# Kernel optimization log

Measured on AMD Instinct MI355X. Metric: run time of the kernel, lower is better.

## Reference

```python
import jax, jax.numpy as jnp
import numpy as np

THRESHOLD = 0.02  # matches init threshold
N_POINTS = 4_000_000
N_PLANES = 64


def setup_inputs() -> dict:
    key = jax.random.key(0)
    k1, k2, k3 = jax.random.split(key, 3)
    points = jax.random.uniform(k1, (N_POINTS, 3), dtype=jnp.float32)
    normals = jax.random.normal(k2, (N_PLANES, 3), dtype=jnp.float32)
    normals = normals / jnp.linalg.norm(normals, axis=1, keepdims=True)
    # anchor each plane at a random point inside the cube so it intersects the cloud
    anchors = jax.random.uniform(k3, (N_PLANES, 3), dtype=jnp.float32)
    distances = jnp.sum(normals * anchors, axis=1)
    return {"points": points, "normals": normals, "distances": distances}


def reference(points, normals, distances):
    """Sequential per-plane SVD refinement + masked projection (faithful to torch loop).

    Plane fits (mask, centroid, covariance) use the ORIGINAL points, as in the
    source; only the projection is applied cumulatively to the running state.
    """
    dtype = points.dtype
    jitter = jnp.diag(jnp.asarray([1.0, 2.0, 3.0], dtype))  # keeps eigh well-posed for invalid planes

    def step(proj, plane):
        n, d = plane
        # inlier mask on original points (data-dependent in torch; here a weight vector)
        m = (jnp.abs(points @ n - d) < THRESHOLD).astype(dtype)  # (N,)
        cnt = jnp.sum(m)
        validf = (cnt >= 3.0).astype(dtype)
        centroid = jnp.sum(m[:, None] * points, axis=0) / jnp.maximum(cnt, 1.0)  # (3,)
        xc = (points - centroid) * m[:, None]  # masked centered points (N,3)
        cov = xc.T @ xc  # (3,3), m is 0/1 so single weighting == mask-select
        cov = cov + (1.0 - validf) * jitter
        # smallest-eigenvalue eigenvector of symmetric cov == torch V[:, 2] (up to sign)
        _, V = jnp.linalg.eigh(cov)
        rn = V[:, 0]
        rn = jnp.where(jnp.dot(rn, n) < 0.0, -rn, rn)  # align with coarse normal
        rd = jnp.dot(centroid, rn)
        # project only masked points of the running state onto refined plane
        delta = (proj @ rn - rd)[:, None] * rn[None, :]  # (N,3)
        proj = proj - (validf * m)[:, None] * delta
        return proj, None

    proj, _ = jax.lax.scan(step, points, (normals, distances))
    return proj
```

## Files before the change

### kernel.cpp

```cpp
#include <hip/hip_runtime.h>
#include <math.h>

#define N_POINTS 4000000
#define N_PLANES 64
#define THRESH   0.02f
#define NVALS    (N_PLANES*10)
#define PPT      12
#define BLKPTS   (PPT*64)
#define NPB      ((N_POINTS + BLKPTS - 1)/BLKPTS)
#define NPAD     (NPB*BLKPTS - N_POINTS)
#define SEG_R    16
#define RBLK     2048
#define RTHR     256

__device__ __forceinline__ float bperm(int addr, float v) {
    return __uint_as_float(__builtin_amdgcn_ds_bpermute(addr, __float_as_uint(v)));
}

__device__ __forceinline__
void load_pts(const float* __restrict__ pts, int pb, int lane,
              float (&X)[PPT], float (&Y)[PPT], float (&Z)[PPT])
{
    const int base = pb * BLKPTS + lane;
    if (pb != NPB - 1) {
#pragma unroll
        for (int u = 0; u < PPT; ++u) {
            const float* P = pts + (long long)(base + u*64) * 3;
            X[u] = P[0]; Y[u] = P[1]; Z[u] = P[2];
        }
    } else {
#pragma unroll
        for (int u = 0; u < PPT; ++u) {
            const int i  = base + u*64;
            const int ic = (i < N_POINTS) ? i : 0;
            const float* P = pts + (long long)ic * 3;
            const float x = P[0], y = P[1], z = P[2];
            const bool v = i < N_POINTS;
            X[u] = v ? x : 0.0f;
            Y[u] = v ? y : 0.0f;
            Z[u] = v ? z : 0.0f;
        }
    }
}

__global__ __launch_bounds__(RTHR, 4)
void reduce_kernel(const float* __restrict__ pts,
                   const float* __restrict__ nrm,
                   const float* __restrict__ dst,
                   float* __restrict__ partials)
{
    const int lane = threadIdx.x & 63;
    const int wid  = threadIdx.x >> 6;

    __shared__ float part[RTHR/64][NVALS];
    for (int v = threadIdx.x; v < (RTHR/64)*NVALS; v += RTHR) (&part[0][0])[v] = 0.f;
    __syncthreads();

    const int rotaddr = ((lane + 1) & 63) << 2;

    int s = wid;
    float cnx, cny, cnz, cnd;
    {
        const int q = (lane + SEG_R * s) & 63;
        cnx = nrm[q*3+0]; cny = nrm[q*3+1]; cnz = nrm[q*3+2]; cnd = -dst[q];
    }

    float PX[PPT], PY[PPT], PZ[PPT], QX[PPT], QY[PPT], QZ[PPT];
    load_pts(pts, blockIdx.x, lane, PX, PY, PZ);

    for (int pb = blockIdx.x; pb < NPB; pb += RBLK) {
        const int pbn = (pb + RBLK < NPB) ? pb + RBLK : pb;
        load_pts(pts, pbn, lane, QX, QY, QZ);

        float a0=0.f,a1=0.f,a2=0.f,a3=0.f,a4=0.f,a5=0.f,a6=0.f,a7=0.f,a8=0.f,a9=0.f;

#pragma unroll 1
        for (int r = 0; r < SEG_R; ++r) {
#pragma unroll
            for (int u = 0; u < PPT; ++u) {
                const float x = PX[u], y = PY[u], z = PZ[u];
                const float t  = fmaf(x, cnx, fmaf(y, cny, fmaf(z, cnz, cnd)));
                const bool  m  = fabsf(t) < THRESH;
                const float fm = m ? 1.0f : 0.0f;
                const float tx = m ? x : 0.0f;
                const float ty = m ? y : 0.0f;
                const float tz = m ? z : 0.0f;
                a0 += fm;
                a1 += tx; a2 += ty; a3 += tz;
                a4 = fmaf(tx, x, a4); a5 = fmaf(tx, y, a5); a6 = fmaf(tx, z, a6);
                a7 = fmaf(ty, y, a7); a8 = fmaf(ty, z, a8); a9 = fmaf(tz, z, a9);
            }
            cnx = bperm(rotaddr, cnx); cny = bperm(rotaddr, cny);
            cnz = bperm(rotaddr, cnz); cnd = bperm(rotaddr, cnd);
            a0 = bperm(rotaddr, a0); a1 = bperm(rotaddr, a1);
            a2 = bperm(rotaddr, a2); a3 = bperm(rotaddr, a3);
            a4 = bperm(rotaddr, a4); a5 = bperm(rotaddr, a5);
            a6 = bperm(rotaddr, a6); a7 = bperm(rotaddr, a7);
            a8 = bperm(rotaddr, a8); a9 = bperm(rotaddr, a9);
        }

        const int wp = (lane + SEG_R * (s + 1)) & 63;
        float* rr = &part[wid][wp * 10];
        rr[0]+=a0; rr[1]+=a1; rr[2]+=a2; rr[3]+=a3; rr[4]+=a4;
        rr[5]+=a5; rr[6]+=a6; rr[7]+=a7; rr[8]+=a8; rr[9]+=a9;

        s = (s + 1) & 3;
#pragma unroll
        for (int u = 0; u < PPT; ++u) { PX[u]=QX[u]; PY[u]=QY[u]; PZ[u]=QZ[u]; }
    }

    __syncthreads();
    for (int v = threadIdx.x; v < NVALS; v += RTHR) {
        float sum = 0.f;
#pragma unroll
        for (int ww = 0; ww < RTHR/64; ++ww) sum += part[ww][v];
        partials[(long long)blockIdx.x * NVALS + v] = sum;
    }
}

__global__ __launch_bounds__(256)
void finalize_kernel(const float* __restrict__ partials, int nb,
                     const float* __restrict__ nrm,
                     const float* __restrict__ dst,
                     float* __restrict__ params)
{
    const int p    = blockIdx.x;
    const int lane = threadIdx.x & 63;
    const int wid  = threadIdx.x >> 6;

    double s[10];
#pragma unroll
    for (int q = 0; q < 10; ++q) s[q] = 0.0;

    for (int b = threadIdx.x; b < nb; b += 256) {
        const float* row = partials + (long long)b * NVALS + p * 10;
#pragma unroll
        for (int q = 0; q < 10; ++q) s[q] += (double)row[q];
    }

#pragma unroll
    for (int off = 32; off; off >>= 1)
#pragma unroll
        for (int q = 0; q < 10; ++q) s[q] += __shfl_xor(s[q], off);

    __shared__ double wsum[4][10];
    if (lane == 0) {
#pragma unroll
        for (int q = 0; q < 10; ++q) wsum[wid][q] = s[q];
    }
    __syncthreads();
    if (threadIdx.x != 0) return;

    double acc[10];
#pragma unroll
    for (int q = 0; q < 10; ++q)
        acc[q] = wsum[0][q] + wsum[1][q] + wsum[2][q] + wsum[3][q];

    double cnt = acc[0];
    if (fabsf(dst[p]) < THRESH) cnt -= (double)NPAD;

    const double sx = acc[1], sy = acc[2], sz = acc[3];
    const double den = fmax(cnt, 1.0);
    const double cx = sx / den, cy = sy / den, cz = sz / den;

    double C[3][3];
    C[0][0] = acc[4] - 2.0*cx*sx + cnt*cx*cx;
    C[0][1] = acc[5] - cx*sy - cy*sx + cnt*cx*cy;
    C[0][2] = acc[6] - cx*sz - cz*sx + cnt*cx*cz;
    C[1][1] = acc[7] - 2.0*cy*sy + cnt*cy*cy;
    C[1][2] = acc[8] - cy*sz - cz*sy + cnt*cy*cz;
    C[2][2] = acc[9] - 2.0*cz*sz + cnt*cz*cz;
    C[1][0] = C[0][1]; C[2][0] = C[0][2]; C[2][1] = C[1][2];

    const double valid = (cnt >= 3.0) ? 1.0 : 0.0;
    C[0][0] += (1.0 - valid) * 1.0;
    C[1][1] += (1.0 - valid) * 2.0;
    C[2][2] += (1.0 - valid) * 3.0;

    double V[3][3] = {{1,0,0},{0,1,0},{0,0,1}};
    for (int sweep = 0; sweep < 15; ++sweep) {
#pragma unroll
        for (int k = 0; k < 3; ++k) {
            const int pp = (k == 2) ? 1 : 0;
            const int qq = (k == 0) ? 1 : 2;
            const int rr = 3 - pp - qq;
            const double apq = C[pp][qq];
            if (fabs(apq) < 1e-300) continue;
            const double theta = (C[qq][qq] - C[pp][pp]) / (2.0 * apq);
            const double t = copysign(1.0, theta) / (fabs(theta) + sqrt(theta*theta + 1.0));
            const double c = 1.0 / sqrt(t*t + 1.0);
            const double ss = t * c;
            const double app = C[pp][pp], aqq = C[qq][qq];
            const double arp = C[rr][pp], arq = C[rr][qq];
            C[pp][pp] = app - t * apq;
            C[qq][qq] = aqq + t * apq;
            C[pp][qq] = 0.0; C[qq][pp] = 0.0;
            const double nrp = c*arp - ss*arq;
            const double nrq = ss*arp + c*arq;
            C[rr][pp] = nrp; C[pp][rr] = nrp;
            C[rr][qq] = nrq; C[qq][rr] = nrq;
#pragma unroll
            for (int i = 0; i < 3; ++i) {
                const double vip = V[i][pp], viq = V[i][qq];
                V[i][pp] = c*vip - ss*viq;
                V[i][qq] = ss*vip + c*viq;
            }
        }
    }

    int idx = 0;
    if (C[1][1] < C[idx][idx]) idx = 1;
    if (C[2][2] < C[idx][idx]) idx = 2;
    double rx = V[0][idx], ry = V[1][idx], rz = V[2][idx];
    const double inv = 1.0 / sqrt(rx*rx + ry*ry + rz*rz);
    rx *= inv; ry *= inv; rz *= inv;

    const double nxd = (double)nrm[p*3+0];
    const double nyd = (double)nrm[p*3+1];
    const double nzd = (double)nrm[p*3+2];
    if (rx*nxd + ry*nyd + rz*nzd < 0.0) { rx = -rx; ry = -ry; rz = -rz; }
    const double rd = cx*rx + cy*ry + cz*rz;

    const float vldf = (float)valid;
    params[p*8+0] = nrm[p*3+0];
    params[p*8+1] = nrm[p*3+1];
    params[p*8+2] = nrm[p*3+2];
    params[p*8+3] = -dst[p];
    params[p*8+4] = vldf * (float)rx;
    params[p*8+5] = vldf * (float)ry;
    params[p*8+6] = vldf * (float)rz;
    params[p*8+7] = -(vldf * (float)rd);
}

#define PPTH 4
#define PQ   (N_POINTS / PPTH)

__global__ __launch_bounds__(256)
void project_kernel(const float* __restrict__ pts,
                    const float* __restrict__ params,
                    float* __restrict__ out)
{
    const int tid = blockIdx.x * 256 + threadIdx.x;
    if (tid >= PQ) return;

    float ox[PPTH], oy[PPTH], oz[PPTH];
    float qx[PPTH], qy[PPTH], qz[PPTH];
#pragma unroll
    for (int k = 0; k < PPTH; ++k) {
        const long long i = (long long)tid + (long long)k * PQ;
        ox[k] = pts[i*3+0]; oy[k] = pts[i*3+1]; oz[k] = pts[i*3+2];
        qx[k] = ox[k]; qy[k] = oy[k]; qz[k] = oz[k];
    }

#pragma unroll 4
    for (int p = 0; p < N_PLANES; ++p) {
        const float nx  = params[p*8+0];
        const float ny  = params[p*8+1];
        const float nz  = params[p*8+2];
        const float md  = params[p*8+3];
        const float rvx = params[p*8+4];
        const float rvy = params[p*8+5];
        const float rvz = params[p*8+6];
        const float mrd = params[p*8+7];

#pragma unroll
        for (int k = 0; k < PPTH; ++k) {
            const float t0 = fmaf(ox[k], nx, fmaf(oy[k], ny, fmaf(oz[k], nz, md)));
            const float t  = fmaf(qx[k], rvx, fmaf(qy[k], rvy, fmaf(qz[k], rvz, mrd)));
            const float tm = (fabsf(t0) < THRESH) ? t : 0.0f;
            qx[k] = fmaf(-tm, rvx, qx[k]);
            qy[k] = fmaf(-tm, rvy, qy[k]);
            qz[k] = fmaf(-tm, rvz, qz[k]);
        }
    }

#pragma unroll
    for (int k = 0; k < PPTH; ++k) {
        const long long i = (long long)tid + (long long)k * PQ;
        out[i*3+0] = qx[k];
        out[i*3+1] = qy[k];
        out[i*3+2] = qz[k];
    }
}

extern "C" void kernel_launch(void* const* d_in, const int* in_sizes, int n_in,
                              void* d_out, int out_size, void* d_ws, size_t ws_size,
                              hipStream_t stream)
{
    const float* pts = (const float*)d_in[0];
    const float* nrm = (const float*)d_in[1];
    const float* dst = (const float*)d_in[2];
    float* out = (float*)d_out;

    float* partials = (float*)d_ws;
    size_t poff = ((size_t)RBLK * NVALS * sizeof(float) + 255) & ~(size_t)255;
    float* params = (float*)((char*)d_ws + poff);

    hipLaunchKernelGGL(reduce_kernel, dim3(RBLK), dim3(RTHR), 0, stream,
                       pts, nrm, dst, partials);
    hipLaunchKernelGGL(finalize_kernel, dim3(N_PLANES), dim3(256), 0, stream,
                       partials, RBLK, nrm, dst, params);
    hipLaunchKernelGGL(project_kernel, dim3((PQ + 255) / 256), dim3(256), 0, stream,
                       pts, params, out);
}
```

Baseline: 186.2 us.

## Restructure reduction to fixed per-block items with persistent rotating accumulators

The reduction kernel now launches 1024 blocks, each processing four contiguous 1024-point chunks with 16 points per lane. The lane accumulators and plane coefficients keep rotating across chunks, so each wave writes its sums to shared memory once with plain stores instead of read-modify-write per chunk, and the shared-memory zeroing pass is dropped. The software prefetch double-buffer is removed, so latency hiding now relies on occupancy. The projection kernel also processes 8 points per thread with a smaller plane-loop unroll, trading registers for more reuse of the plane parameters.

```diff
diff --git a/kernel.cpp b/kernel.cpp
--- a/kernel.cpp
+++ b/kernel.cpp
@@ -5,42 +5,18 @@
 #define N_PLANES 64
 #define THRESH   0.02f
 #define NVALS    (N_PLANES*10)
-#define PPT      12
+#define PPT      16
 #define BLKPTS   (PPT*64)
-#define NPB      ((N_POINTS + BLKPTS - 1)/BLKPTS)
+#define G1       1024
+#define ITEMS    4
+#define NPB      (G1*ITEMS)
 #define NPAD     (NPB*BLKPTS - N_POINTS)
+#define FULL_PB  (N_POINTS/BLKPTS)
 #define SEG_R    16
-#define RBLK     2048
 #define RTHR     256
 
 __device__ __forceinline__ float bperm(int addr, float v) {
     return __uint_as_float(__builtin_amdgcn_ds_bpermute(addr, __float_as_uint(v)));
-}
-
-__device__ __forceinline__
-void load_pts(const float* __restrict__ pts, int pb, int lane,
-              float (&X)[PPT], float (&Y)[PPT], float (&Z)[PPT])
-{
-    const int base = pb * BLKPTS + lane;
-    if (pb != NPB - 1) {
-#pragma unroll
-        for (int u = 0; u < PPT; ++u) {
-            const float* P = pts + (long long)(base + u*64) * 3;
-            X[u] = P[0]; Y[u] = P[1]; Z[u] = P[2];
-        }
-    } else {
-#pragma unroll
-        for (int u = 0; u < PPT; ++u) {
-            const int i  = base + u*64;
-            const int ic = (i < N_POINTS) ? i : 0;
-            const float* P = pts + (long long)ic * 3;
-            const float x = P[0], y = P[1], z = P[2];
-            const bool v = i < N_POINTS;
-            X[u] = v ? x : 0.0f;
-            Y[u] = v ? y : 0.0f;
-            Z[u] = v ? z : 0.0f;
-        }
-    }
 }
 
 __global__ __launch_bounds__(RTHR, 4)
@@ -53,26 +29,37 @@
     const int wid  = threadIdx.x >> 6;
 
     __shared__ float part[RTHR/64][NVALS];
-    for (int v = threadIdx.x; v < (RTHR/64)*NVALS; v += RTHR) (&part[0][0])[v] = 0.f;
-    __syncthreads();
 
     const int rotaddr = ((lane + 1) & 63) << 2;
 
-    int s = wid;
     float cnx, cny, cnz, cnd;
     {
-        const int q = (lane + SEG_R * s) & 63;
+        const int q = (lane + SEG_R * wid) & 63;
         cnx = nrm[q*3+0]; cny = nrm[q*3+1]; cnz = nrm[q*3+2]; cnd = -dst[q];
     }
 
-    float PX[PPT], PY[PPT], PZ[PPT], QX[PPT], QY[PPT], QZ[PPT];
-    load_pts(pts, blockIdx.x, lane, PX, PY, PZ);
-
-    for (int pb = blockIdx.x; pb < NPB; pb += RBLK) {
-        const int pbn = (pb + RBLK < NPB) ? pb + RBLK : pb;
-        load_pts(pts, pbn, lane, QX, QY, QZ);
-
-        float a0=0.f,a1=0.f,a2=0.f,a3=0.f,a4=0.f,a5=0.f,a6=0.f,a7=0.f,a8=0.f,a9=0.f;
+    float a0=0.f,a1=0.f,a2=0.f,a3=0.f,a4=0.f,a5=0.f,a6=0.f,a7=0.f,a8=0.f,a9=0.f;
+    float PX[PPT], PY[PPT], PZ[PPT];
+
+    for (int it = 0; it < ITEMS; ++it) {
+        const int pb = blockIdx.x * ITEMS + it;
+
+        const float* P0 = pts + ((size_t)pb * BLKPTS + lane) * 3;
+        if (pb < FULL_PB) {
+#pragma unroll
+            for (int u = 0; u < PPT; ++u) {
+                PX[u] = P0[u*192+0]; PY[u] = P0[u*192+1]; PZ[u] = P0[u*192+2];
+            }
+        } else if (pb == FULL_PB) {
+#pragma unroll
+            for (int u = 0; u < PPT; ++u) {
+                if (u < 4) { PX[u] = P0[u*192+0]; PY[u] = P0[u*192+1]; PZ[u] = P0[u*192+2]; }
+                else       { PX[u] = 0.f; PY[u] = 0.f; PZ[u] = 0.f; }
+            }
+        } else {
+#pragma unroll
+            for (int u = 0; u < PPT; ++u) { PX[u] = 0.f; PY[u] = 0.f; PZ[u] = 0.f; }
+        }
 
 #pragma unroll 1
         for (int r = 0; r < SEG_R; ++r) {
@@ -98,17 +85,14 @@
             a6 = bperm(rotaddr, a6); a7 = bperm(rotaddr, a7);
             a8 = bperm(rotaddr, a8); a9 = bperm(rotaddr, a9);
         }
-
-        const int wp = (lane + SEG_R * (s + 1)) & 63;
+    }
+
+    {
+        const int wp = (lane + SEG_R * wid) & 63;
         float* rr = &part[wid][wp * 10];
-        rr[0]+=a0; rr[1]+=a1; rr[2]+=a2; rr[3]+=a3; rr[4]+=a4;
-        rr[5]+=a5; rr[6]+=a6; rr[7]+=a7; rr[8]+=a8; rr[9]+=a9;
-
-        s = (s + 1) & 3;
-#pragma unroll
-        for (int u = 0; u < PPT; ++u) { PX[u]=QX[u]; PY[u]=QY[u]; PZ[u]=QZ[u]; }
-    }
-
+        rr[0]=a0; rr[1]=a1; rr[2]=a2; rr[3]=a3; rr[4]=a4;
+        rr[5]=a5; rr[6]=a6; rr[7]=a7; rr[8]=a8; rr[9]=a9;
+    }
     __syncthreads();
     for (int v = threadIdx.x; v < NVALS; v += RTHR) {
         float sum = 0.f;
@@ -232,7 +216,7 @@
     params[p*8+7] = -(vldf * (float)rd);
 }
 
-#define PPTH 4
+#define PPTH 8
 #define PQ   (N_POINTS / PPTH)
 
 __global__ __launch_bounds__(256)
@@ -252,7 +236,7 @@
         qx[k] = ox[k]; qy[k] = oy[k]; qz[k] = oz[k];
     }
 
-#pragma unroll 4
+#pragma unroll 2
     for (int p = 0; p < N_PLANES; ++p) {
         const float nx  = params[p*8+0];
         const float ny  = params[p*8+1];
@@ -293,13 +277,13 @@
     float* out = (float*)d_out;
 
     float* partials = (float*)d_ws;
-    size_t poff = ((size_t)RBLK * NVALS * sizeof(float) + 255) & ~(size_t)255;
+    size_t poff = ((size_t)G1 * NVALS * sizeof(float) + 255) & ~(size_t)255;
     float* params = (float*)((char*)d_ws + poff);
 
-    hipLaunchKernelGGL(reduce_kernel, dim3(RBLK), dim3(RTHR), 0, stream,
+    hipLaunchKernelGGL(reduce_kernel, dim3(G1), dim3(RTHR), 0, stream,
                        pts, nrm, dst, partials);
     hipLaunchKernelGGL(finalize_kernel, dim3(N_PLANES), dim3(256), 0, stream,
-                       partials, RBLK, nrm, dst, params);
+                       partials, G1, nrm, dst, params);
     hipLaunchKernelGGL(project_kernel, dim3((PQ + 255) / 256), dim3(256), 0, stream,
                        pts, params, out);
 }
```

New measurement: 197.0 us. +5.8%, slower.
